# Kernel tuning notes

Hardware: AMD Instinct MI355X
Metric: run time of the kernel (lower is better)

## Reference

```python
import jax, jax.numpy as jnp
import numpy as np

D = 64        # GatedGraphConv out_channels
N_LAYERS = 5  # number of stacked convs


def setup_inputs() -> dict:
    key = jax.random.key(0)
    ks = jax.random.split(key, 16)
    N, E, G = 100000, 1600000, 64
    s = 0.1
    inp = {
        'conv_weight': jax.random.normal(ks[0], (N_LAYERS, D, D), jnp.float32) * s,
        'gru_w_ih':    jax.random.normal(ks[1], (N_LAYERS, 3 * D, D), jnp.float32) * s,
        'gru_w_hh':    jax.random.normal(ks[2], (N_LAYERS, 3 * D, D), jnp.float32) * s,
        'gru_b_ih':    jax.random.normal(ks[3], (N_LAYERS, 3 * D), jnp.float32) * s,
        'gru_b_hh':    jax.random.normal(ks[4], (N_LAYERS, 3 * D), jnp.float32) * s,
        'fc1_w': jax.random.normal(ks[5], (32, D), jnp.float32) * s,
        'fc1_b': jax.random.normal(ks[6], (32,), jnp.float32) * s,
        'fc2_w': jax.random.normal(ks[7], (16, 32), jnp.float32) * s,
        'fc2_b': jax.random.normal(ks[8], (16,), jnp.float32) * s,
        'fc3_w': jax.random.normal(ks[9], (1, 16), jnp.float32) * s,
        'fc3_b': jax.random.normal(ks[10], (1,), jnp.float32) * s,
        'edge_index': jax.random.randint(ks[11], (2, E), 0, N, jnp.int64 if jax.config.jax_enable_x64 else jnp.int32),
        'batch': jnp.sort(jax.random.randint(ks[12], (N,), 0, G, jnp.int32)),
        'num_nodes': N,
        'num_graphs': G,
    }
    return inp


def _gru_cell(m, h, w_ih, w_hh, b_ih, b_hh):
    # torch.nn.GRUCell math; m: [N,D] input, h: [N,D] hidden
    gi = m @ w_ih.T + b_ih   # [N, 3D]
    gh = h @ w_hh.T + b_hh   # [N, 3D]
    i_r, i_z, i_n = jnp.split(gi, 3, axis=1)
    h_r, h_z, h_n = jnp.split(gh, 3, axis=1)
    r = jax.nn.sigmoid(i_r + h_r)
    z = jax.nn.sigmoid(i_z + h_z)
    n = jnp.tanh(i_n + r * h_n)
    return (1.0 - z) * n + z * h


def reference(conv_weight, gru_w_ih, gru_w_hh, gru_b_ih, gru_b_hh,
              fc1_w, fc1_b, fc2_w, fc2_b, fc3_w, fc3_b,
              edge_index, batch, num_nodes, num_graphs):
    src, dst = edge_index[0], edge_index[1]  # source_to_target flow
    # initial node features: zeros [N,8] zero-padded to D by GatedGraphConv
    x0 = jnp.zeros((num_nodes, D), jnp.float32)

    def step(x, params):
        w, wih, whh, bih, bhh = params
        m = x @ w                                        # [N, D]
        agg = jax.ops.segment_sum(m[src], dst, num_segments=num_nodes)  # scatter-add
        return _gru_cell(agg, x, wih, whh, bih, bhh), None

    x, _ = jax.lax.scan(step, x0,
                        (conv_weight, gru_w_ih, gru_w_hh, gru_b_ih, gru_b_hh))

    # scatter_add pooling over batch -> [num_graphs, D]
    g = jax.ops.segment_sum(x, batch, num_segments=num_graphs)
    h = jax.nn.elu(g @ fc1_w.T + fc1_b)
    h = jax.nn.elu(h @ fc2_w.T + fc2_b)
    return h @ fc3_w.T + fc3_b  # [num_graphs, 1]
```

## Files before the change

kernel.cpp:

```cpp
#include <hip/hip_runtime.h>
#include <math.h>

typedef _Float16 f16x2 __attribute__((ext_vector_type(2)));
typedef _Float16 f16x4 __attribute__((ext_vector_type(4)));
typedef _Float16 f16x8 __attribute__((ext_vector_type(8)));
typedef float f32x4 __attribute__((ext_vector_type(4)));

#define CBITS 10
#define FCHUNK 4096
#define MATSZ 13056
__device__ __forceinline__ int woff(int row) { return 64 * row + 8 * (row >> 1); }

__device__ __forceinline__ float sigmoidf_(float v) {
  return 1.0f / (1.0f + __expf(-v));
}
__device__ __forceinline__ float tanhf_(float v) {
  v = fminf(fmaxf(v, -15.f), 15.f);
  float e = __expf(2.f * v);
  return (e - 1.f) / (e + 1.f);
}
__device__ __forceinline__ float eluf_(float v) { return v > 0.f ? v : (__expf(v) - 1.f); }

__global__ __launch_bounds__(256) void fuse_w_kernel(const float* __restrict__ conv_w,
                                                     const float* __restrict__ w_ih,
                                                     _Float16* __restrict__ wcS) {
  const int l = blockIdx.x >> 2;
  const int j0 = (blockIdx.x & 3) * 48;
  const float* W = conv_w + (size_t)l * 4096;
  const float* wi = w_ih + (size_t)l * 12288;
  _Float16* out = wcS + (size_t)l * MATSZ;
  __shared__ float sWt[64 * 68];
  __shared__ float sI[48 * 64];
  const int t = threadIdx.x;
  for (int i = t; i < 4096; i += 256) sWt[(i & 63) * 68 + (i >> 6)] = W[i];
  for (int i = t; i < 3072; i += 256) sI[i] = wi[j0 * 64 + i];
  __syncthreads();
#pragma unroll
  for (int r = 0; r < 3; ++r) {
    int u = t + 256 * r;
    int j = u >> 4, cg = (u & 15) * 4;
    float4 a = {0.f, 0.f, 0.f, 0.f};
    for (int k = 0; k < 64; ++k) {
      float4 w = *(const float4*)(sWt + k * 68 + cg);
      float s = sI[j * 64 + k];
      a.x += w.x * s; a.y += w.y * s; a.z += w.z * s; a.w += w.w * s;
    }
    int row = j0 + j;
    f16x4 hv;
    hv[0] = (_Float16)a.x; hv[1] = (_Float16)a.y;
    hv[2] = (_Float16)a.z; hv[3] = (_Float16)a.w;
    *(f16x4*)(out + woff(row) + cg) = hv;
  }
}

__global__ __launch_bounds__(256) void whh_prep_kernel(const float* __restrict__ whh,
                                                       _Float16* __restrict__ whhS) {
  int idx = blockIdx.x * 256 + threadIdx.x;
  if (idx >= 15360) return;
  int l = idx / 3072, rem = idx % 3072;
  int r = rem >> 4, c4 = (rem & 15) * 4;
  float4 v = *(const float4*)(whh + (size_t)l * 12288 + r * 64 + c4);
  f16x4 hv;
  hv[0] = (_Float16)v.x; hv[1] = (_Float16)v.y;
  hv[2] = (_Float16)v.z; hv[3] = (_Float16)v.w;
  *(f16x4*)(whhS + (size_t)l * MATSZ + woff(r) + c4) = hv;
}

__global__ __launch_bounds__(256) void bucket_hist_kernel(const int* __restrict__ dst,
                                                          int* __restrict__ bh, int E) {
  __shared__ int h[128];
  const int t = threadIdx.x;
  if (t < 128) h[t] = 0;
  __syncthreads();
  for (int e = blockIdx.x * 256 + t; e < E; e += gridDim.x * 256)
    atomicAdd(&h[dst[e] >> CBITS], 1);
  __syncthreads();
  if (t < 128 && h[t]) atomicAdd(&bh[t * 16], h[t]);
}

__global__ __launch_bounds__(128) void bucket_scan_kernel(int* __restrict__ bh, int nbk,
                                                          int* __restrict__ boffs, int E,
                                                          float* __restrict__ gbuf, int gn) {
  __shared__ int s[128];
  const int t = threadIdx.x;
  for (int i = t; i < gn; i += 128) gbuf[i] = 0.f;
  int v = (t < nbk) ? bh[t * 16] : 0;
  s[t] = v;
  __syncthreads();
  for (int o = 1; o < 128; o <<= 1) {
    int a = (t >= o) ? s[t - o] : 0;
    __syncthreads();
    s[t] += a;
    __syncthreads();
  }
  if (t < nbk) {
    int ex = s[t] - v;
    boffs[t] = ex;
    bh[t * 16] = ex;
  }
  if (t == 0) boffs[nbk] = E;
}

__global__ __launch_bounds__(256) void bucket_fill_kernel(const int* __restrict__ src,
                                                          const int* __restrict__ dst,
                                                          int* __restrict__ bcur,
                                                          unsigned* __restrict__ pairs, int E) {
  __shared__ uint2 staged[FCHUNK];
  __shared__ int h[128], lbase[128], gbase[128], lcur[128];
  const int t = threadIdx.x;
  const int e0 = blockIdx.x * FCHUNK;
  int cnt = E - e0;
  if (cnt > FCHUNK) cnt = FCHUNK;
  if (t < 128) h[t] = 0;
  __syncthreads();
  for (int i = t; i < cnt; i += 256) atomicAdd(&h[dst[e0 + i] >> CBITS], 1);
  __syncthreads();
  if (t < 128) lcur[t] = h[t];
  __syncthreads();
  for (int o = 1; o < 128; o <<= 1) {
    int a = 0;
    if (t < 128 && t >= o) a = lcur[t - o];
    __syncthreads();
    if (t < 128) lcur[t] += a;
    __syncthreads();
  }
  if (t < 128) {
    int ex = lcur[t] - h[t];
    lbase[t] = ex;
    if (h[t]) gbase[t] = atomicAdd(&bcur[t * 16], h[t]);
    lcur[t] = ex;
  }
  __syncthreads();
  for (int i = t; i < cnt; i += 256) {
    int d = dst[e0 + i];
    int b = d >> CBITS;
    int p = atomicAdd(&lcur[b], 1);
    staged[p] = make_uint2((unsigned)src[e0 + i], (unsigned)d);
  }
  __syncthreads();
  for (int i = t; i < cnt; i += 256) {
    uint2 pr = staged[i];
    int b = (int)(pr.y >> CBITS);
    pairs[gbase[b] + (i - lbase[b])] = (pr.x << CBITS) | (pr.y & ((1u << CBITS) - 1));
  }
}

__global__ __launch_bounds__(256) void csr_build_kernel(const unsigned* __restrict__ pairs,
                                                        const int* __restrict__ boffs,
                                                        int* __restrict__ offs,
                                                        int* __restrict__ srcs, int N, int E) {
  const int b = blockIdx.x, t = threadIdx.x;
  const int nbase = b << CBITS;
  __shared__ int deg[1024];
  __shared__ int ssc[256];
  for (int i = t; i < 1024; i += 256) deg[i] = 0;
  __syncthreads();
  const int beg = boffs[b], end = boffs[b + 1];
  for (int e = beg + t; e < end; e += 256) atomicAdd(&deg[pairs[e] & 1023], 1);
  __syncthreads();
  int d0 = deg[4 * t], d1 = deg[4 * t + 1], d2 = deg[4 * t + 2], d3 = deg[4 * t + 3];
  int s = d0 + d1 + d2 + d3;
  ssc[t] = s;
  __syncthreads();
  for (int o = 1; o < 256; o <<= 1) {
    int a = (t >= o) ? ssc[t - o] : 0;
    __syncthreads();
    ssc[t] += a;
    __syncthreads();
  }
  int base = beg + ssc[t] - s;
  int c0 = base, c1 = c0 + d0, c2 = c1 + d1, c3 = c2 + d2;
  if (nbase + 4 * t + 0 < N) offs[nbase + 4 * t + 0] = c0;
  if (nbase + 4 * t + 1 < N) offs[nbase + 4 * t + 1] = c1;
  if (nbase + 4 * t + 2 < N) offs[nbase + 4 * t + 2] = c2;
  if (nbase + 4 * t + 3 < N) offs[nbase + 4 * t + 3] = c3;
  deg[4 * t] = c0; deg[4 * t + 1] = c1; deg[4 * t + 2] = c2; deg[4 * t + 3] = c3;
  if (b == 0 && t == 0) offs[N] = E;
  if (b == 0 && t < 64) srcs[E + t] = 0;
  __syncthreads();
  for (int e = beg + t; e < end; e += 256) {
    unsigned p = pairs[e];
    int pos = atomicAdd(&deg[p & 1023], 1);
    srcs[pos] = (int)(p >> CBITS);
  }
}

__global__ __launch_bounds__(256) void l01_prep_kernel(const float* __restrict__ b_ih0,
                                                       const float* __restrict__ b_hh0,
                                                       const _Float16* __restrict__ wcS1,
                                                       const _Float16* __restrict__ whhS1,
                                                       const float* __restrict__ b_ih1,
                                                       const float* __restrict__ b_hh1,
                                                       float* __restrict__ h1,
                                                       float* __restrict__ u,
                                                       float* __restrict__ cons) {
  __shared__ float sh1[64];
  int j = threadIdx.x;
  if (j < 64) {
    float r = sigmoidf_(b_ih0[j] + b_hh0[j]);
    float z = sigmoidf_(b_ih0[64 + j] + b_hh0[64 + j]);
    float n = tanhf_(b_ih0[128 + j] + r * b_hh0[128 + j]);
    float h = (1.f - z) * n;
    sh1[j] = h;
    h1[j] = h;
  }
  __syncthreads();
  if (j >= 192) return;
  float su = 0.f, sg = 0.f;
  const int base = woff(j);
  for (int c = 0; c < 64; ++c) {
    float hc = sh1[c];
    su += hc * (float)wcS1[base + c];
    sg += hc * (float)whhS1[base + c];
  }
  u[j] = su;
  if (j < 128) {
    cons[j] = sg + b_ih1[j] + b_hh1[j];
  } else {
    cons[j] = b_ih1[j];
    cons[j + 64] = sg + b_hh1[j];
  }
}

__global__ __launch_bounds__(256) void l1_elem_kernel(const int* __restrict__ offs,
                                                      const float* __restrict__ h1,
                                                      const float* __restrict__ u,
                                                      const float* __restrict__ cons,
                                                      _Float16* __restrict__ xh,
                                                      int N, int units) {
  int idx = blockIdx.x * 256 + threadIdx.x;
  if (idx >= units) return;
  int v = idx >> 5, lp = idx & 31;
  float dg = (v < N) ? (float)(offs[v + 1] - offs[v]) : 0.f;
  f16x2 o;
#pragma unroll
  for (int k = 0; k < 2; ++k) {
    int d = 2 * lp + k;
    float r = sigmoidf_(dg * u[d] + cons[d]);
    float z = sigmoidf_(dg * u[64 + d] + cons[64 + d]);
    float n = tanhf_(dg * u[128 + d] + cons[128 + d] + r * cons[192 + d]);
    o[k] = (_Float16)(n + z * (h1[d] - n));
  }
  *(f16x2*)(xh + (size_t)idx * 2) = o;
}

__global__ __launch_bounds__(256) void agg_kernel(const _Float16* __restrict__ xh,
                                                  const int* __restrict__ offs,
                                                  const int* __restrict__ srcs,
                                                  _Float16* __restrict__ aggh, int N) {
  int wave = threadIdx.x >> 6, lane = threadIdx.x & 63;
  int v = blockIdx.x * 4 + wave;
  if (v >= N) return;
  const int beg = offs[v], end = offs[v + 1];
  const int deg = end - beg;
  const int og = lane >> 3;
  const int lp = lane & 7;
  f16x8 acc = {};
  for (int base = 0; base < deg; base += 64) {
    const int cnt = min(64, deg - base);
    int sidx = srcs[beg + base + lane];
    for (int e = 0; e < cnt; e += 8) {
      int me = e + og;
      int s = __shfl(sidx, me);
      f16x8 vv = *(const f16x8*)(xh + (size_t)s * 64 + lp * 8);
      if (me < cnt) acc += vv;
    }
  }
#pragma unroll
  for (int off = 8; off < 64; off <<= 1) {
    union { f16x8 h; int i[4]; } a, b;
    a.h = acc;
#pragma unroll
    for (int w = 0; w < 4; ++w) b.i[w] = __shfl_xor(a.i[w], off);
    acc += b.h;
  }
  if (og == 0) *(f16x8*)(aggh + (size_t)v * 64 + lp * 8) = acc;
}

__global__ __launch_bounds__(256) void gru_kernel(const _Float16* __restrict__ aggh,
                                                  const _Float16* __restrict__ xh_in,
                                                  _Float16* __restrict__ xh_out,
                                                  const _Float16* __restrict__ wcS,
                                                  const _Float16* __restrict__ whhS,
                                                  const float* __restrict__ b_ih,
                                                  const float* __restrict__ b_hh,
                                                  int N, int numIter) {
  const int t = threadIdx.x;
  const int wave = t >> 6, lane = t & 63;
  const int q = lane >> 4, c = lane & 15;
  float bRZ[4], bZZ[4], bIN[4], bHN[4];
#pragma unroll
  for (int dt = 0; dt < 4; ++dt) {
    int d = dt * 16 + c;
    bRZ[dt] = b_ih[d] + b_hh[d];
    bZZ[dt] = b_ih[64 + d] + b_hh[64 + d];
    bIN[dt] = b_ih[128 + d];
    bHN[dt] = b_hh[128 + d];
  }
  f16x8 idf[2];
#pragma unroll
  for (int p = 0; p < 2; ++p) {
    int tgt = p * 16 + c - q * 8;
#pragma unroll
    for (int j = 0; j < 8; ++j) idf[p][j] = (j == tgt) ? (_Float16)1.0f : (_Float16)0.0f;
  }
#pragma unroll 1
  for (int it = blockIdx.x; it < numIter; it += gridDim.x) {
    const int tile = it >> 1, half = it & 1;
    const int nb0 = tile * 64 + wave * 16;
    const size_t rowbase = (size_t)(nb0 + c) * 64;
    f16x8 aA[2], aH[2];
#pragma unroll
    for (int ks = 0; ks < 2; ++ks) {
      aA[ks] = *(const f16x8*)(aggh + rowbase + ks * 32 + q * 8);
      aH[ks] = *(const f16x8*)(xh_in + rowbase + ks * 32 + q * 8);
    }
    f32x4 aR[2], aZ[2], aN[2], aHNa[2], aHO[2];
#pragma unroll
    for (int p = 0; p < 2; ++p) {
      float brz = half ? bRZ[2 + p] : bRZ[p];
      float bzz = half ? bZZ[2 + p] : bZZ[p];
      float bin = half ? bIN[2 + p] : bIN[p];
      float bhn = half ? bHN[2 + p] : bHN[p];
      aR[p] = (f32x4){brz, brz, brz, brz};
      aZ[p] = (f32x4){bzz, bzz, bzz, bzz};
      aN[p] = (f32x4){bin, bin, bin, bin};
      aHNa[p] = (f32x4){bhn, bhn, bhn, bhn};
      aHO[p] = (f32x4){0.f, 0.f, 0.f, 0.f};
    }
#pragma unroll
    for (int ks = 0; ks < 2; ++ks) {
      const int colo = ks * 32 + q * 8;
#pragma unroll
      for (int p = 0; p < 2; ++p) {
        const int r0 = (half * 2 + p) * 16 + c;
        f16x8 bWr = *(const f16x8*)(wcS + woff(r0) + colo);
        f16x8 bHr = *(const f16x8*)(whhS + woff(r0) + colo);
        f16x8 bWz = *(const f16x8*)(wcS + woff(64 + r0) + colo);
        f16x8 bHz = *(const f16x8*)(whhS + woff(64 + r0) + colo);
        f16x8 bWn = *(const f16x8*)(wcS + woff(128 + r0) + colo);
        f16x8 bHn = *(const f16x8*)(whhS + woff(128 + r0) + colo);
        aR[p] = __builtin_amdgcn_mfma_f32_16x16x32_f16(aA[ks], bWr, aR[p], 0, 0, 0);
        aR[p] = __builtin_amdgcn_mfma_f32_16x16x32_f16(aH[ks], bHr, aR[p], 0, 0, 0);
        aZ[p] = __builtin_amdgcn_mfma_f32_16x16x32_f16(aA[ks], bWz, aZ[p], 0, 0, 0);
        aZ[p] = __builtin_amdgcn_mfma_f32_16x16x32_f16(aH[ks], bHz, aZ[p], 0, 0, 0);
        aN[p] = __builtin_amdgcn_mfma_f32_16x16x32_f16(aA[ks], bWn, aN[p], 0, 0, 0);
        aHNa[p] = __builtin_amdgcn_mfma_f32_16x16x32_f16(aH[ks], bHn, aHNa[p], 0, 0, 0);
      }
    }
#pragma unroll
    for (int p = 0; p < 2; ++p)
      aHO[p] = __builtin_amdgcn_mfma_f32_16x16x32_f16(aH[half], idf[p], aHO[p], 0, 0, 0);
#pragma unroll
    for (int p = 0; p < 2; ++p) {
      int d = (half * 2 + p) * 16 + c;
#pragma unroll
      for (int r = 0; r < 4; ++r) {
        int node = nb0 + q * 4 + r;
        if (node < N) {
          float rr = sigmoidf_(aR[p][r]);
          float zz = sigmoidf_(aZ[p][r]);
          float nn = tanhf_(aN[p][r] + rr * aHNa[p][r]);
          float out = nn + zz * (aHO[p][r] - nn);
          xh_out[(size_t)node * 64 + d] = (_Float16)out;
        }
      }
    }
  }
}

__global__ __launch_bounds__(256) void pool_kernel(const _Float16* __restrict__ xh,
                                                   const int* __restrict__ batch,
                                                   float* __restrict__ g, int N) {
  int wave = threadIdx.x >> 6, lane = threadIdx.x & 63;
  int n0 = blockIdx.x * 64 + wave * 16;
  if (n0 >= N) return;
  int end = n0 + 16;
  if (end > N) end = N;
  int cur = batch[n0];
  float acc = 0.f;
  for (int n = n0; n < end; ++n) {
    int b = batch[n];
    if (b != cur) {
      atomicAdd(&g[(size_t)cur * 64 + lane], acc);
      acc = 0.f;
      cur = b;
    }
    acc += (float)xh[(size_t)n * 64 + lane];
  }
  atomicAdd(&g[(size_t)cur * 64 + lane], acc);
}

__global__ __launch_bounds__(256) void mlp_kernel(const float* __restrict__ g,
                                                  const float* __restrict__ w1,
                                                  const float* __restrict__ b1,
                                                  const float* __restrict__ w2,
                                                  const float* __restrict__ b2,
                                                  const float* __restrict__ w3,
                                                  const float* __restrict__ b3,
                                                  float* __restrict__ out, int G) {
  __shared__ float sG[64 * 64];
  __shared__ float sH1[64 * 32];
  __shared__ float sH2[64 * 16];
  int t = threadIdx.x;
  for (int i = t; i < G * 64; i += 256) sG[i] = g[i];
  __syncthreads();
  for (int o = t; o < G * 32; o += 256) {
    int gi = o >> 5, i = o & 31;
    float a = b1[i];
    for (int k = 0; k < 64; ++k) a += sG[gi * 64 + k] * w1[i * 64 + k];
    sH1[gi * 32 + i] = eluf_(a);
  }
  __syncthreads();
  for (int o = t; o < G * 16; o += 256) {
    int gi = o >> 4, i = o & 15;
    float a = b2[i];
    for (int k = 0; k < 32; ++k) a += sH1[gi * 32 + k] * w2[i * 32 + k];
    sH2[gi * 16 + i] = eluf_(a);
  }
  __syncthreads();
  for (int o = t; o < G; o += 256) {
    float a = b3[0];
    for (int k = 0; k < 16; ++k) a += sH2[o * 16 + k] * w3[k];
    out[o] = a;
  }
}

extern "C" void kernel_launch(void* const* d_in, const int* in_sizes, int n_in,
                              void* d_out, int out_size, void* d_ws, size_t ws_size,
                              hipStream_t stream) {
  const float* conv_w = (const float*)d_in[0];
  const float* w_ih = (const float*)d_in[1];
  const float* w_hh = (const float*)d_in[2];
  const float* b_ih = (const float*)d_in[3];
  const float* b_hh = (const float*)d_in[4];
  const float* fc1_w = (const float*)d_in[5];
  const float* fc1_b = (const float*)d_in[6];
  const float* fc2_w = (const float*)d_in[7];
  const float* fc2_b = (const float*)d_in[8];
  const float* fc3_w = (const float*)d_in[9];
  const float* fc3_b = (const float*)d_in[10];
  const int* ei = (const int*)d_in[11];
  const int* batch = (const int*)d_in[12];
  const int N = in_sizes[12];
  const int E = in_sizes[11] / 2;
  const int G = out_size;
  const int* src = ei;
  const int* dst = ei + E;
  const int nbk = (N + 1023) >> CBITS;
  const int tiles = (N + 63) / 64;
  const int Npad = tiles * 64;
  const int gruIter = tiles * 2;

  char* ws = (char*)d_ws;
  size_t off = 0;
  auto alloc = [&](size_t bytes) -> void* {
    void* p = ws + off;
    off += (bytes + 255) & ~(size_t)255;
    return p;
  };
  _Float16* xhA = (_Float16*)alloc((size_t)Npad * 64 * 2);
  _Float16* xhB = (_Float16*)alloc((size_t)Npad * 64 * 2);
  _Float16* aggh = (_Float16*)alloc((size_t)Npad * 64 * 2);
  _Float16* wcS = (_Float16*)alloc((size_t)5 * MATSZ * 2);
  _Float16* whhS = (_Float16*)alloc((size_t)5 * MATSZ * 2);
  float* h1 = (float*)alloc(64 * 4);
  float* l1u = (float*)alloc(192 * 4);
  float* l1c = (float*)alloc(256 * 4);
  float* gbuf = (float*)alloc((size_t)G * 64 * 4);
  int* offs = (int*)alloc((size_t)(N + 1) * 4);
  int* srcs = (int*)alloc((size_t)(E + 64) * 4);
  unsigned* pairs = (unsigned*)alloc((size_t)E * 4);
  int* bh = (int*)alloc(128 * 16 * 4);
  int* boffs = (int*)alloc(129 * 4);

  hipMemsetAsync(bh, 0, 128 * 16 * 4, stream);
  bucket_hist_kernel<<<256, 256, 0, stream>>>(dst, bh, E);
  bucket_scan_kernel<<<1, 128, 0, stream>>>(bh, nbk, boffs, E, gbuf, G * 64);
  bucket_fill_kernel<<<(E + FCHUNK - 1) / FCHUNK, 256, 0, stream>>>(src, dst, bh, pairs, E);
  csr_build_kernel<<<nbk, 256, 0, stream>>>(pairs, boffs, offs, srcs, N, E);

  fuse_w_kernel<<<20, 256, 0, stream>>>(conv_w, w_ih, wcS);
  whh_prep_kernel<<<60, 256, 0, stream>>>(w_hh, whhS);

  l01_prep_kernel<<<1, 256, 0, stream>>>(b_ih, b_hh, wcS + MATSZ, whhS + MATSZ,
                                         b_ih + 192, b_hh + 192, h1, l1u, l1c);
  l1_elem_kernel<<<(Npad * 32 + 255) / 256, 256, 0, stream>>>(offs, h1, l1u, l1c, xhA,
                                                              N, Npad * 32);

  _Float16* cur = xhA;
  _Float16* nxt = xhB;
  for (int l = 2; l < 5; ++l) {
    agg_kernel<<<(N + 3) / 4, 256, 0, stream>>>(cur, offs, srcs, aggh, N);
    gru_kernel<<<gruIter, 256, 0, stream>>>(aggh, cur, nxt, wcS + (size_t)l * MATSZ,
                                            whhS + (size_t)l * MATSZ, b_ih + (size_t)l * 192,
                                            b_hh + (size_t)l * 192, N, gruIter);
    _Float16* tmp = cur; cur = nxt; nxt = tmp;
  }

  pool_kernel<<<(N + 63) / 64, 256, 0, stream>>>(cur, batch, gbuf, N);
  mlp_kernel<<<1, 256, 0, stream>>>(gbuf, fc1_w, fc1_b, fc2_w, fc2_b, fc3_w, fc3_b,
                                    (float*)d_out, G);
}
```

Measured before the change: 469.6 us.

## Stage GRU weight halves in LDS and use persistent grid-stride blocks

Each GRU block now works on one fixed output half. At launch it copies that half's six weight segments (W and Whh for r, z, n) into shared memory, then loops over node tiles with a grid stride from a fixed grid of 768 blocks. This replaces the per-tile global/L2 loads of the weight fragments with LDS reads, and the weight staging cost is paid once per block. The trade-offs are extra shared memory per block and the fixed grid size, which could lower occupancy or balance.

```diff
diff --git a/kernel.cpp b/kernel.cpp
--- a/kernel.cpp
+++ b/kernel.cpp
@@ -9,6 +9,7 @@
 #define CBITS 10
 #define FCHUNK 4096
 #define MATSZ 13056
+#define SEGSZ 2176
 __device__ __forceinline__ int woff(int row) { return 64 * row + 8 * (row >> 1); }
 
 __device__ __forceinline__ float sigmoidf_(float v) {
@@ -284,18 +285,29 @@
                                                   const _Float16* __restrict__ whhS,
                                                   const float* __restrict__ b_ih,
                                                   const float* __restrict__ b_hh,
-                                                  int N, int numIter) {
+                                                  int N, int tiles) {
+  __shared__ _Float16 sW[2 * 3 * SEGSZ];
   const int t = threadIdx.x;
+  const int half = blockIdx.x & 1;
+  for (int i = t; i < 1632; i += 256) {
+    int mat = (i >= 816) ? 1 : 0;
+    int rem = i - mat * 816;
+    int seg = rem / 272;
+    int u = rem % 272;
+    const _Float16* srcp = (mat ? whhS : wcS) + woff(half * 32 + seg * 64) + u * 8;
+    *(f16x8*)(sW + (mat * 3 + seg) * SEGSZ + u * 8) = *(const f16x8*)srcp;
+  }
+  __syncthreads();
   const int wave = t >> 6, lane = t & 63;
   const int q = lane >> 4, c = lane & 15;
-  float bRZ[4], bZZ[4], bIN[4], bHN[4];
-#pragma unroll
-  for (int dt = 0; dt < 4; ++dt) {
-    int d = dt * 16 + c;
-    bRZ[dt] = b_ih[d] + b_hh[d];
-    bZZ[dt] = b_ih[64 + d] + b_hh[64 + d];
-    bIN[dt] = b_ih[128 + d];
-    bHN[dt] = b_hh[128 + d];
+  float bRZ[2], bZZ[2], bIN[2], bHN[2];
+#pragma unroll
+  for (int p = 0; p < 2; ++p) {
+    int d = (half * 2 + p) * 16 + c;
+    bRZ[p] = b_ih[d] + b_hh[d];
+    bZZ[p] = b_ih[64 + d] + b_hh[64 + d];
+    bIN[p] = b_ih[128 + d];
+    bHN[p] = b_hh[128 + d];
   }
   f16x8 idf[2];
 #pragma unroll
@@ -305,8 +317,7 @@
     for (int j = 0; j < 8; ++j) idf[p][j] = (j == tgt) ? (_Float16)1.0f : (_Float16)0.0f;
   }
 #pragma unroll 1
-  for (int it = blockIdx.x; it < numIter; it += gridDim.x) {
-    const int tile = it >> 1, half = it & 1;
+  for (int tile = blockIdx.x >> 1; tile < tiles; tile += gridDim.x >> 1) {
     const int nb0 = tile * 64 + wave * 16;
     const size_t rowbase = (size_t)(nb0 + c) * 64;
     f16x8 aA[2], aH[2];
@@ -318,14 +329,10 @@
     f32x4 aR[2], aZ[2], aN[2], aHNa[2], aHO[2];
 #pragma unroll
     for (int p = 0; p < 2; ++p) {
-      float brz = half ? bRZ[2 + p] : bRZ[p];
-      float bzz = half ? bZZ[2 + p] : bZZ[p];
-      float bin = half ? bIN[2 + p] : bIN[p];
-      float bhn = half ? bHN[2 + p] : bHN[p];
-      aR[p] = (f32x4){brz, brz, brz, brz};
-      aZ[p] = (f32x4){bzz, bzz, bzz, bzz};
-      aN[p] = (f32x4){bin, bin, bin, bin};
-      aHNa[p] = (f32x4){bhn, bhn, bhn, bhn};
+      aR[p] = (f32x4){bRZ[p], bRZ[p], bRZ[p], bRZ[p]};
+      aZ[p] = (f32x4){bZZ[p], bZZ[p], bZZ[p], bZZ[p]};
+      aN[p] = (f32x4){bIN[p], bIN[p], bIN[p], bIN[p]};
+      aHNa[p] = (f32x4){bHN[p], bHN[p], bHN[p], bHN[p]};
       aHO[p] = (f32x4){0.f, 0.f, 0.f, 0.f};
     }
 #pragma unroll
@@ -333,13 +340,14 @@
       const int colo = ks * 32 + q * 8;
 #pragma unroll
       for (int p = 0; p < 2; ++p) {
-        const int r0 = (half * 2 + p) * 16 + c;
-        f16x8 bWr = *(const f16x8*)(wcS + woff(r0) + colo);
-        f16x8 bHr = *(const f16x8*)(whhS + woff(r0) + colo);
-        f16x8 bWz = *(const f16x8*)(wcS + woff(64 + r0) + colo);
-        f16x8 bHz = *(const f16x8*)(whhS + woff(64 + r0) + colo);
-        f16x8 bWn = *(const f16x8*)(wcS + woff(128 + r0) + colo);
-        f16x8 bHn = *(const f16x8*)(whhS + woff(128 + r0) + colo);
+        const int lr = p * 16 + c;
+        const int ro = 64 * lr + 8 * (lr >> 1);
+        f16x8 bWr = *(const f16x8*)(sW + 0 * SEGSZ + ro + colo);
+        f16x8 bWz = *(const f16x8*)(sW + 1 * SEGSZ + ro + colo);
+        f16x8 bWn = *(const f16x8*)(sW + 2 * SEGSZ + ro + colo);
+        f16x8 bHr = *(const f16x8*)(sW + 3 * SEGSZ + ro + colo);
+        f16x8 bHz = *(const f16x8*)(sW + 4 * SEGSZ + ro + colo);
+        f16x8 bHn = *(const f16x8*)(sW + 5 * SEGSZ + ro + colo);
         aR[p] = __builtin_amdgcn_mfma_f32_16x16x32_f16(aA[ks], bWr, aR[p], 0, 0, 0);
         aR[p] = __builtin_amdgcn_mfma_f32_16x16x32_f16(aH[ks], bHr, aR[p], 0, 0, 0);
         aZ[p] = __builtin_amdgcn_mfma_f32_16x16x32_f16(aA[ks], bWz, aZ[p], 0, 0, 0);
@@ -450,7 +458,6 @@
   const int nbk = (N + 1023) >> CBITS;
   const int tiles = (N + 63) / 64;
   const int Npad = tiles * 64;
-  const int gruIter = tiles * 2;
 
   char* ws = (char*)d_ws;
   size_t off = 0;
@@ -492,9 +499,9 @@
   _Float16* nxt = xhB;
   for (int l = 2; l < 5; ++l) {
     agg_kernel<<<(N + 3) / 4, 256, 0, stream>>>(cur, offs, srcs, aggh, N);
-    gru_kernel<<<gruIter, 256, 0, stream>>>(aggh, cur, nxt, wcS + (size_t)l * MATSZ,
-                                            whhS + (size_t)l * MATSZ, b_ih + (size_t)l * 192,
-                                            b_hh + (size_t)l * 192, N, gruIter);
+    gru_kernel<<<768, 256, 0, stream>>>(aggh, cur, nxt, wcS + (size_t)l * MATSZ,
+                                        whhS + (size_t)l * MATSZ, b_ih + (size_t)l * 192,
+                                        b_hh + (size_t)l * 192, N, tiles);
     _Float16* tmp = cur; cur = nxt; nxt = tmp;
   }
 
```

Measured after the change: 413.5 us. -12.0%, faster.
